# Performance work log

Hardware: AMD Instinct MI355X
Metric: run time of the kernel (lower is better)

Reference implementation:

```python
import jax, jax.numpy as jnp
import numpy as np

N = 50000          # nodes
E = 1_600_000      # edges
R = 16             # num_relations
NB = 4             # num_bases
FIN = 128          # num_node_features
H = 128            # hidden_channels
G = 64             # num graphs in batch
NC = 2             # num_classes


def rgcn_conv(x, edge_index, edge_type, bases, comp, root, bias):
    """PyG RGCNConv with basis decomposition, mean aggregation per relation."""
    n = x.shape[0]
    # weight[r] = sum_b comp[r,b] * bases[b]  -> [R, in, out]
    weight = jnp.einsum('rb,bio->rio', comp, bases)
    src, dst = edge_index[0], edge_index[1]
    # segment id combining destination node and relation
    seg = dst * R + edge_type                      # [E]
    msg = x[src]                                   # [E, in] gather
    summed = jax.ops.segment_sum(msg, seg, num_segments=n * R)      # [N*R, in]
    cnt = jax.ops.segment_sum(jnp.ones((msg.shape[0],), x.dtype), seg,
                              num_segments=n * R)                   # [N*R]
    mean = summed / jnp.maximum(cnt, 1.0)[:, None]
    mean = mean.reshape(n, R, -1)                  # [N, R, in]
    out = jnp.einsum('nri,rio->no', mean, weight) + x @ root + bias
    return out


def global_mean_pool(x, batch, num_graphs):
    s = jax.ops.segment_sum(x, batch, num_segments=num_graphs)
    c = jax.ops.segment_sum(jnp.ones((x.shape[0],), x.dtype), batch,
                            num_segments=num_graphs)
    return s / jnp.maximum(c, 1.0)[:, None]


def setup_inputs() -> dict:
    key = jax.random.key(0)
    ks = jax.random.split(key, 24)
    inp = {
        'x': jax.random.normal(ks[0], (N, FIN), jnp.float32),
        'edge_index': jax.random.randint(ks[1], (2, E), 0, N),
        'edge_type': jax.random.randint(ks[2], (E,), 0, R),
        'batch': jnp.sort(jax.random.randint(ks[3], (N,), 0, G)),
        'rel_labels': jax.random.randint(ks[4], (G,), 0, R),
        'drop_prob': 0,
        'rel_emb': jax.random.normal(ks[5], (R, H), jnp.float32),
    }
    s1 = 1.0 / np.sqrt(FIN)
    s2 = 1.0 / np.sqrt(H)
    inp['bases1'] = jax.random.normal(ks[6], (NB, FIN, H), jnp.float32) * s1
    inp['comp1'] = jax.random.normal(ks[7], (R, NB), jnp.float32)
    inp['root1'] = jax.random.normal(ks[8], (FIN, H), jnp.float32) * s1
    inp['bias1'] = jnp.zeros((H,), jnp.float32)
    inp['bases2'] = jax.random.normal(ks[9], (NB, H, H), jnp.float32) * s2
    inp['comp2'] = jax.random.normal(ks[10], (R, NB), jnp.float32)
    inp['root2'] = jax.random.normal(ks[11], (H, H), jnp.float32) * s2
    inp['bias2'] = jnp.zeros((H,), jnp.float32)
    inp['bases3'] = jax.random.normal(ks[12], (NB, H, H), jnp.float32) * s2
    inp['comp3'] = jax.random.normal(ks[13], (R, NB), jnp.float32)
    inp['root3'] = jax.random.normal(ks[14], (H, H), jnp.float32) * s2
    inp['bias3'] = jnp.zeros((H,), jnp.float32)
    inp['lin_w'] = jax.random.normal(ks[15], (2 * H, NC), jnp.float32) * (1.0 / np.sqrt(2 * H))
    inp['lin_b'] = jnp.zeros((NC,), jnp.float32)
    return inp


def reference(x, edge_index, edge_type, batch, rel_labels, drop_prob, rel_emb,
              bases1, comp1, root1, bias1,
              bases2, comp2, root2, bias2,
              bases3, comp3, root3, bias3,
              lin_w, lin_b):
    rel_embs = rel_emb[rel_labels]                               # [G, H]
    h = jax.nn.relu(rgcn_conv(x, edge_index, edge_type, bases1, comp1, root1, bias1))
    h = jax.nn.relu(rgcn_conv(h, edge_index, edge_type, bases2, comp2, root2, bias2))
    h = rgcn_conv(h, edge_index, edge_type, bases3, comp3, root3, bias3)
    pooled = global_mean_pool(h, batch, G)                       # [G, H]
    z = jnp.concatenate([pooled, rel_embs], axis=1)              # [G, 2H]
    # dropout with p=drop_prob in eval mode (reference is deterministic) -> identity
    return z @ lin_w + lin_b                                     # [G, NC]
```

## Files before the change

kernel.cpp:

```cpp
#include <hip/hip_runtime.h>

#define NN 50000
#define EE 1600000
#define RR 16
#define NBASE 4
#define FINF 128
#define HD 128
#define NG 64
#define NCLS 2
#define NRSEG (NN*RR)

typedef __attribute__((ext_vector_type(8))) short short8;
typedef __attribute__((ext_vector_type(4))) float f32x4;
typedef __attribute__((ext_vector_type(2))) float f32x2;
typedef unsigned short u16;
typedef unsigned int u32;
typedef unsigned long long u64;
typedef unsigned char u8;

__device__ __forceinline__ float bflo(u32 u){ return __builtin_bit_cast(float, u << 16); }
__device__ __forceinline__ float bfhi(u32 u){ return __builtin_bit_cast(float, u & 0xFFFF0000u); }
__device__ __forceinline__ u16 f2bf(float f){
  u32 u = __builtin_bit_cast(u32, f);
  u += 0x7FFFu + ((u >> 16) & 1u);
  return (u16)(u >> 16);
}
__device__ __forceinline__ u32 cvt_pk_bf16(float a, float b){
  u32 r;
  asm("v_cvt_pk_bf16_f32 %0, %1, %2" : "=v"(r) : "v"(a), "v"(b));
  return r;
}
__device__ __forceinline__ float fastrcp(float x){
#if __has_builtin(__builtin_amdgcn_rcpf)
  return __builtin_amdgcn_rcpf(x);
#else
  return 1.0f / x;
#endif
}
__device__ __forceinline__ float ldf(const void* p, int i, int isbf){
  return isbf ? bflo((u32)((const u16*)p)[i]) : ((const float*)p)[i];
}

__device__ __forceinline__ float fp8_manual(u32 b){
  u32 s = (b>>7)&1, e = (b>>3)&15, m = b&7;
  float v;
  if (e==0) v = (float)m * 0.001953125f;
  else      v = __builtin_bit_cast(float, ((e+120u)<<23) | (m<<20));
  return s ? -v : v;
}
__device__ __forceinline__ u32 f32_to_fp8_manual(float f){
  u32 u = __builtin_bit_cast(u32, f);
  u32 s = u>>31;
  int e = (int)((u>>23)&0xFF);
  u32 m = u & 0x7FFFFF;
  int ee = e - 120;
  if (ee <= 0) return s<<7;
  u32 m3 = m >> 20, rem = m & 0xFFFFF;
  u32 rnd = (rem > 0x80000u) || (rem == 0x80000u && (m3 & 1));
  m3 += rnd;
  if (m3 == 8){ m3 = 0; ee += 1; }
  if (ee >= 16){ ee = 15; m3 = 6; }
  return (s<<7) | ((u32)ee<<3) | m3;
}
__device__ __forceinline__ void fp8x2_to_f32(u32 v, float& a, float& b){
#if __has_builtin(__builtin_amdgcn_cvt_pk_f32_fp8)
  f32x2 r = __builtin_amdgcn_cvt_pk_f32_fp8((int)v, false);
  a = r[0]; b = r[1];
#else
  a = fp8_manual(v & 0xFF); b = fp8_manual((v>>8)&0xFF);
#endif
}
__device__ __forceinline__ u32 pk_fp8x2(float a, float b){
  a = fminf(fmaxf(a, -448.f), 448.f);
  b = fminf(fmaxf(b, -448.f), 448.f);
#if __has_builtin(__builtin_amdgcn_cvt_pk_fp8_f32)
  return (u32)__builtin_amdgcn_cvt_pk_fp8_f32(a, b, 0, false) & 0xFFFF;
#else
  return f32_to_fp8_manual(a) | (f32_to_fp8_manual(b) << 8);
#endif
}

__global__ void k_detect(const u32* __restrict__ xw, int* __restrict__ flag){
  __shared__ int votes;
  if (threadIdx.x == 0) votes = 0;
  __syncthreads();
  u32 w = xw[threadIdx.x];
  int e = (w >> 7) & 0xFF;
  if (e >= 100 && e <= 129) atomicAdd(&votes, 1);
  __syncthreads();
  if (threadIdx.x == 0) flag[0] = (votes >= 192) ? 1 : 0;
}

__global__ void k_quant(const void* __restrict__ src, u8* __restrict__ dstq,
                        const int* __restrict__ flagp, int* __restrict__ cnt){
  int i = blockIdx.x*256 + threadIdx.x;
  if (i < NRSEG) cnt[i] = 0;
  if (i >= NN*HD/4) return;
  int isbf = flagp[0];
  float v0,v1,v2,v3;
  if (isbf){
    u32 a = ((const u32*)src)[i*2+0], b = ((const u32*)src)[i*2+1];
    v0=bflo(a); v1=bfhi(a); v2=bflo(b); v3=bfhi(b);
  } else {
    float4 f = ((const float4*)src)[i];
    v0=f.x; v1=f.y; v2=f.z; v3=f.w;
  }
  u32 q = pk_fp8x2(v0,v1) | (pk_fp8x2(v2,v3) << 16);
  ((u32*)dstq)[i] = q;
}


__global__ void k_hist(const int* __restrict__ dst, const int* __restrict__ et,
                       int* __restrict__ cnt){
  int e = blockIdx.x*256 + threadIdx.x;
  if (e < EE) atomicAdd(&cnt[et[e]*NN + dst[e]], 1);
}

#define SCB 1024
__global__ __launch_bounds__(SCB) void k_scan1(const int* __restrict__ cnt,
                                               int* __restrict__ off,
                                               int* __restrict__ bsum){
  __shared__ int sh[SCB];
  int tid = threadIdx.x;
  int i = blockIdx.x*SCB + tid;
  int v = (i < NRSEG) ? cnt[i] : 0;
  sh[tid] = v; __syncthreads();
  for (int d=1; d<SCB; d<<=1){
    int t = (tid >= d) ? sh[tid-d] : 0;
    __syncthreads();
    sh[tid] += t;
    __syncthreads();
  }
  if (i < NRSEG) off[i] = sh[tid] - v;
  if (tid == SCB-1) bsum[blockIdx.x] = sh[SCB-1];
}

__global__ __launch_bounds__(1024) void k_scan2(int* __restrict__ bsum, int nb){
  __shared__ int sh[1024];
  __shared__ int carry;
  int tid = threadIdx.x;
  if (tid == 0) carry = 0;
  __syncthreads();
  for (int base=0; base<nb; base+=1024){
    int i = base + tid;
    int v = (i < nb) ? bsum[i] : 0;
    int orig = v;
    sh[tid] = v; __syncthreads();
    for (int d=1; d<1024; d<<=1){
      int t = (tid >= d) ? sh[tid-d] : 0;
      __syncthreads();
      sh[tid] += t;
      __syncthreads();
    }
    int total = sh[1023];
    int excl = sh[tid] - orig + carry;
    if (i < nb) bsum[i] = excl;
    __syncthreads();
    if (tid == 0) carry += total;
    __syncthreads();
  }
}

__global__ __launch_bounds__(SCB) void k_scan3(const int* __restrict__ cnt,
                                               int* __restrict__ off,
                                               const int* __restrict__ bsum){
  int i = blockIdx.x*SCB + threadIdx.x;
  if (i < NRSEG){
    int o = off[i] + bsum[blockIdx.x];
    off[i] = o;
    if (i == NRSEG-1) off[NRSEG] = o + cnt[i];
  }
}

__global__ void k_scatter(const int* __restrict__ src, const int* __restrict__ dst,
                          const int* __restrict__ et, const int* __restrict__ off,
                          int* __restrict__ cnt, int* __restrict__ esrc){
  int e = blockIdx.x*256 + threadIdx.x;
  if (e < EE){
    int seg = et[e]*NN + dst[e];
    int p = atomicSub(&cnt[seg], 1) - 1;
    esrc[off[seg] + p] = src[e] << 7;
  }
}


__global__ void k_weights3(const void* __restrict__ b0, const void* __restrict__ c0,
                           const void* __restrict__ r0,
                           const void* __restrict__ b1, const void* __restrict__ c1,
                           const void* __restrict__ r1,
                           const void* __restrict__ b2, const void* __restrict__ c2,
                           const void* __restrict__ r2,
                           u16* __restrict__ WTf, const int* __restrict__ flagp){
  int gid = blockIdx.x;
  int layer = gid / 1088;
  int blk = gid - layer*1088;
  int idx = blk*256 + threadIdx.x;
  if (idx >= 17*16384) return;
  const void* bases = (layer==0) ? b0 : (layer==1) ? b1 : b2;
  const void* comp  = (layer==0) ? c0 : (layer==1) ? c1 : c2;
  const void* root  = (layer==0) ? r0 : (layer==1) ? r1 : r2;
  u16* W = WTf + (u32)layer * (17*16384);
  int isbf = flagp[0];
  int r = idx >> 14;
  int o = (idx >> 7) & 127;
  int i = idx & 127;
  float v;
  if (r < RR){
    v = 0.f;
    #pragma unroll
    for (int b=0;b<NBASE;b++)
      v += ldf(comp, r*NBASE+b, isbf) * ldf(bases, (b*FINF + i)*HD + o, isbf);
  } else {
    v = ldf(root, i*HD + o, isbf);
  }
  int wv = o >> 5, ct = (o >> 4) & 1, mrow = o & 15;
  int ks = i >> 5, quad = (i >> 3) & 3, j = i & 7;
  int lane = quad*16 + mrow;
  W[(u32)((((r*4+wv)*2+ct)*4+ks)*64 + lane)*8 + j] = f2bf(v);
}


#define TN 32

#define GLD(rg, ei) { u32 voff_ = (u32)__builtin_amdgcn_readlane(eiv, (ei)) + lane2u; \
  asm volatile("global_load_ushort %0, %1, %2" : "=v"(rg) : "v"(voff_), "s"(xq)); }
#define WAITV0 { asm volatile("s_waitcnt vmcnt(0)" ::: "memory"); \
  __builtin_amdgcn_sched_barrier(0); }
#define CNS(rg, k) if ((k) < cnt){ int eg_ = sbeg + (k); \
  while (idx < TN && nbv <= eg_) doflush(); \
  float da_, db_; fp8x2_to_f32(rg, da_, db_); a0 += da_; a1 += db_; }

__global__ __launch_bounds__(256, 4) void k_layer(
    const u8*  __restrict__ xq,
    const u16* __restrict__ WTf,
    const void* __restrict__ bias, const int* __restrict__ off,
    const int* __restrict__ esrc,
    u16* __restrict__ hout,
    u8* __restrict__ hq,
    const int* __restrict__ flagp, int write_bf, int relu)
{
  __shared__ __align__(16) u16 Abuf[4][TN*136];
  __shared__ int soff[RR*(TN+1)];
  int tid = threadIdx.x;
  int n0 = blockIdx.x * TN;
  int isbf_in = flagp[0];

  int wv = tid >> 6;
  int lane = tid & 63;
  u32 lane2u = (u32)(lane << 1);
  int mrow = lane & 15;
  int quad = lane >> 4;

  for (int i = tid; i < RR*(TN+1); i += 256){
    int r = i / (TN+1), k = i - r*(TN+1);
    int n = n0 + k; if (n > NN) n = NN;
    soff[i] = off[r*NN + n];
  }
  __syncthreads();

  f32x4 acc[2][2];
  { f32x4 z = {0.f,0.f,0.f,0.f};
    acc[0][0]=z; acc[0][1]=z; acc[1][0]=z; acc[1][1]=z; }

  for (int t=0; t<4; ++t){
    int r = t*4 + wv;
    {
      int offv = 0;
      if (lane <= TN) offv = soff[r*(TN+1) + lane];
      int wstart = __builtin_amdgcn_readlane(offv, 0);
      int wend   = __builtin_amdgcn_readlane(offv, TN);
      int blen = wend - wstart;

      float a0 = 0.f, a1 = 0.f;
      int idx = 0;
      int cb = wstart;
      int nbv = __builtin_amdgcn_readlane(offv, 1);
      u16* abase = Abuf[wv] + lane*2;

      auto doflush = [&](){
        int cnt_ = nbv - cb;
        float cf = (float)(cnt_ > 0 ? cnt_ : 1);
        float inv = fastrcp(cf);
        *(u32*)(abase + idx*136) = cvt_pk_bf16(a0*inv, a1*inv);
        a0 = 0.f; a1 = 0.f;
        cb = nbv; idx++;
        if (idx < TN) nbv = __builtin_amdgcn_readlane(offv, idx+1);
      };

      if (blen > 0 && blen <= 128){
        int c0 = blen - 1;
        int eiv0 = esrc[wstart + (lane < c0 ? lane : c0)];
        int eiv1 = 0;
        if (blen > 64){
          int c1 = blen - 65;
          eiv1 = esrc[wstart + 64 + (lane < c1 ? lane : c1)];
        }

        auto batch32 = [&](int eiv, int lb, int sbeg, int cnt)
            __attribute__((always_inline)) {
          u32 r0,r1,r2,r3,r4,r5,r6,r7,r8,r9,r10,r11,r12,r13,r14,r15,
              r16,r17,r18,r19,r20,r21,r22,r23,r24,r25,r26,r27,r28,r29,r30,r31;
          GLD(r0, lb+0) GLD(r1, lb+1) GLD(r2, lb+2) GLD(r3, lb+3)
          GLD(r4, lb+4) GLD(r5, lb+5) GLD(r6, lb+6) GLD(r7, lb+7)
          if (cnt > 8){
            GLD(r8, lb+8)  GLD(r9, lb+9)  GLD(r10, lb+10) GLD(r11, lb+11)
            GLD(r12, lb+12) GLD(r13, lb+13) GLD(r14, lb+14) GLD(r15, lb+15)
          }
          if (cnt > 16){
            GLD(r16, lb+16) GLD(r17, lb+17) GLD(r18, lb+18) GLD(r19, lb+19)
            GLD(r20, lb+20) GLD(r21, lb+21) GLD(r22, lb+22) GLD(r23, lb+23)
          }
          if (cnt > 24){
            GLD(r24, lb+24) GLD(r25, lb+25) GLD(r26, lb+26) GLD(r27, lb+27)
            GLD(r28, lb+28) GLD(r29, lb+29) GLD(r30, lb+30) GLD(r31, lb+31)
          }
          WAITV0
          CNS(r0, 0) CNS(r1, 1) CNS(r2, 2) CNS(r3, 3)
          CNS(r4, 4) CNS(r5, 5) CNS(r6, 6) CNS(r7, 7)
          CNS(r8, 8) CNS(r9, 9) CNS(r10, 10) CNS(r11, 11)
          CNS(r12, 12) CNS(r13, 13) CNS(r14, 14) CNS(r15, 15)
          CNS(r16, 16) CNS(r17, 17) CNS(r18, 18) CNS(r19, 19)
          CNS(r20, 20) CNS(r21, 21) CNS(r22, 22) CNS(r23, 23)
          CNS(r24, 24) CNS(r25, 25) CNS(r26, 26) CNS(r27, 27)
          CNS(r28, 28) CNS(r29, 29) CNS(r30, 30) CNS(r31, 31)
        };

        int cnt0 = blen < 64 ? blen : 64;
        int cA = cnt0 < 32 ? cnt0 : 32;
        batch32(eiv0, 0, wstart, cA);
        if (cnt0 > 32) batch32(eiv0, 32, wstart + 32, cnt0 - 32);
        if (blen > 64){
          int cnt1 = blen - 64;
          int cB = cnt1 < 32 ? cnt1 : 32;
          batch32(eiv1, 0, wstart + 64, cB);
          if (cnt1 > 32) batch32(eiv1, 32, wstart + 96, cnt1 - 32);
        }
      } else if (blen > 0){
        for (int e = wstart; e < wend; ++e){
          int sid = __builtin_amdgcn_readfirstlane(esrc[e]);
          while (idx < TN && nbv <= e) doflush();
          float da, db;
          fp8x2_to_f32((u32)*(const u16*)(xq + (u32)sid + lane2u), da, db);
          a0 += da; a1 += db;
        }
      }
      while (idx < TN) doflush();
    }
    __syncthreads();
    #pragma unroll
    for (int rloc=0; rloc<4; ++rloc){
      int rr = t*4 + rloc;
      const u16* Bp = WTf + (u32)(((rr*4 + wv)*2)*4*64)*8 + (u32)lane*8;
      short8 bf[2][4];
      #pragma unroll
      for (int ct=0; ct<2; ++ct)
        #pragma unroll
        for (int ks=0; ks<4; ++ks)
          bf[ct][ks] = *(const short8*)(Bp + (u32)(ct*4 + ks)*64*8);
      #pragma unroll
      for (int mt=0; mt<2; ++mt){
        #pragma unroll
        for (int ks=0; ks<4; ++ks){
          short8 af = *(const short8*)(Abuf[rloc] + (mt*16 + mrow)*136 + ks*32 + quad*8);
          #pragma unroll
          for (int ct=0; ct<2; ++ct)
            acc[mt][ct] = __builtin_amdgcn_mfma_f32_16x16x32_bf16(af, bf[ct][ks], acc[mt][ct], 0, 0, 0);
        }
      }
    }
    __syncthreads();
  }
  {
    const u16* Bp = WTf + (u32)(((16*4 + wv)*2)*4*64)*8 + (u32)lane*8;
    short8 bf[2][4];
    #pragma unroll
    for (int ct=0; ct<2; ++ct)
      #pragma unroll
      for (int ks=0; ks<4; ++ks)
        bf[ct][ks] = *(const short8*)(Bp + (u32)(ct*4 + ks)*64*8);
    #pragma unroll
    for (int mt=0; mt<2; ++mt){
      const u8* xrow = xq + (u32)(n0 + mt*16 + mrow)*HD;
      #pragma unroll
      for (int ks=0; ks<4; ++ks){
        u32 lo = *(const u32*)(xrow + ks*32 + quad*8);
        u32 hi = *(const u32*)(xrow + ks*32 + quad*8 + 4);
        float f0,f1,f2,f3,f4,f5,f6,f7;
        fp8x2_to_f32(lo & 0xFFFFu, f0, f1);
        fp8x2_to_f32(lo >> 16,     f2, f3);
        fp8x2_to_f32(hi & 0xFFFFu, f4, f5);
        fp8x2_to_f32(hi >> 16,     f6, f7);
        union { short8 v; u32 w[4]; } u;
        u.w[0] = cvt_pk_bf16(f0,f1); u.w[1] = cvt_pk_bf16(f2,f3);
        u.w[2] = cvt_pk_bf16(f4,f5); u.w[3] = cvt_pk_bf16(f6,f7);
        #pragma unroll
        for (int ct=0; ct<2; ++ct)
          acc[mt][ct] = __builtin_amdgcn_mfma_f32_16x16x32_bf16(u.v, bf[ct][ks], acc[mt][ct], 0, 0, 0);
      }
    }
  }
  #pragma unroll
  for (int mt=0; mt<2; ++mt){
    #pragma unroll
    for (int ct=0; ct<2; ++ct){
      int col = wv*32 + ct*16 + mrow;
      float bv = ldf(bias, col, isbf_in);
      #pragma unroll
      for (int rg=0; rg<4; ++rg){
        int n = n0 + mt*16 + quad*4 + rg;
        if (n < NN){
          float v = acc[mt][ct][rg] + bv;
          if (relu) v = fmaxf(v, 0.f);
          if (!(v == v)) v = 0.f;
          if (write_bf) hout[(u32)(n*HD + col)] = f2bf(v);
          else          hq[(u32)(n*HD + col)] = (u8)(pk_fp8x2(v, 0.f) & 0xFF);
        }
      }
    }
  }
}


__global__ __launch_bounds__(1024) void k_pool_head(
    const u16* __restrict__ h, const int* __restrict__ batch,
    const int* __restrict__ rlab, const void* __restrict__ rel_emb,
    const void* __restrict__ lin_w, const void* __restrict__ lin_b,
    void* __restrict__ out, const int* __restrict__ flagp)
{
  int g = blockIdx.x;
  int isbf = flagp[0];
  __shared__ int bounds[2];
  __shared__ float psum[8][128];
  __shared__ float red[4];
  if (threadIdx.x == 0){
    int lo=0, hi=NN;
    while (lo < hi){ int m=(lo+hi)>>1; if (batch[m] < g) lo=m+1; else hi=m; }
    bounds[0] = lo;
    int lo2=lo, hi2=NN;
    while (lo2 < hi2){ int m=(lo2+hi2)>>1; if (batch[m] < g+1) lo2=m+1; else hi2=m; }
    bounds[1] = lo2;
  }
  __syncthreads();
  int lo = bounds[0], hi = bounds[1];
  int f = threadIdx.x & 127;
  int s = threadIdx.x >> 7;
  float acc = 0.f;
  for (int n = lo + s; n < hi; n += 8) acc += bflo((u32)h[(u32)(n*HD + f)]);
  psum[s][f] = acc;
  __syncthreads();
  if (threadIdx.x < 128){
    int cn = hi - lo;
    float tot = 0.f;
    #pragma unroll
    for (int k=0;k<8;k++) tot += psum[k][f];
    float pooled = tot / (float)(cn > 0 ? cn : 1);
    int rl = rlab[g];
    float re = ldf(rel_emb, rl*HD + f, isbf);
    float v0 = pooled * ldf(lin_w, f*NCLS+0, isbf) + re * ldf(lin_w, (HD+f)*NCLS+0, isbf);
    float v1 = pooled * ldf(lin_w, f*NCLS+1, isbf) + re * ldf(lin_w, (HD+f)*NCLS+1, isbf);
    #pragma unroll
    for (int o=32;o>0;o>>=1){ v0 += __shfl_down(v0,o); v1 += __shfl_down(v1,o); }
    int ln = threadIdx.x & 63, wvv = threadIdx.x >> 6;
    if (ln == 0){ red[wvv*2] = v0; red[wvv*2+1] = v1; }
  }
  __syncthreads();
  if (threadIdx.x == 0){
    float o0 = red[0] + red[2] + ldf(lin_b, 0, isbf);
    float o1 = red[1] + red[3] + ldf(lin_b, 1, isbf);
    if (isbf){
      ((u16*)out)[g*NCLS+0] = f2bf(o0);
      ((u16*)out)[g*NCLS+1] = f2bf(o1);
    } else {
      ((float*)out)[g*NCLS+0] = o0;
      ((float*)out)[g*NCLS+1] = o1;
    }
  }
}


extern "C" void kernel_launch(void* const* d_in, const int* in_sizes, int n_in,
                              void* d_out, int out_size, void* d_ws, size_t ws_size,
                              hipStream_t stream)
{
  (void)in_sizes; (void)n_in; (void)out_size; (void)ws_size;
  const void* x      = d_in[0];
  const int* eidx    = (const int*)d_in[1];
  const int* etype   = (const int*)d_in[2];
  const int* batch   = (const int*)d_in[3];
  const int* rlab    = (const int*)d_in[4];
  const void* rel_emb = d_in[6];
  const void* basesA[3] = {d_in[7],  d_in[11], d_in[15]};
  const void* compA[3]  = {d_in[8],  d_in[12], d_in[16]};
  const void* rootA[3]  = {d_in[9],  d_in[13], d_in[17]};
  const void* biasA[3]  = {d_in[10], d_in[14], d_in[18]};
  const void* lin_w  = d_in[19];
  const void* lin_b  = d_in[20];

  char* p = (char*)d_ws;
  auto alloc = [&](size_t bytes)->char*{ char* r = p; p += (bytes + 255) & ~(size_t)255; return r; };
  int*   flag   = (int*)  alloc(256);
  int*   off    = (int*)  alloc((size_t)(NRSEG+1)*4);
  int*   esrc   = (int*)  alloc((size_t)(EE+64)*4);
  u16*   WTf    = (u16*)  alloc((size_t)3*17*16384*2);
  u8*    xq     = (u8*)   alloc((size_t)NN*HD);
  u8*    h1q    = (u8*)   alloc((size_t)NN*HD);
  u8*    h2q    = (u8*)   alloc((size_t)NN*HD);
  u16*   h3     = (u16*)  alloc((size_t)NN*HD*2);
  int*   cnt    = (int*)h3;
  int*   bsum   = (int*)((char*)h3 + (size_t)NRSEG*4);

  const int* src_in = eidx;
  const int* dst_in = eidx + EE;

  const int nscan = (NRSEG + SCB - 1) / SCB;

  k_detect <<<1, 256, 0, stream>>>((const u32*)x, flag);
  k_quant  <<<(NN*HD/4 + 255)/256, 256, 0, stream>>>(x, xq, flag, cnt);
  k_hist   <<<EE/256, 256, 0, stream>>>(dst_in, etype, cnt);
  k_scan1  <<<nscan, SCB, 0, stream>>>(cnt, off, bsum);
  k_scan2  <<<1,    1024, 0, stream>>>(bsum, nscan);
  k_scan3  <<<nscan, SCB, 0, stream>>>(cnt, off, bsum);
  k_scatter<<<EE/256, 256, 0, stream>>>(src_in, dst_in, etype, off, cnt, esrc);

  k_weights3<<<3*1088, 256, 0, stream>>>(basesA[0], compA[0], rootA[0],
                                         basesA[1], compA[1], rootA[1],
                                         basesA[2], compA[2], rootA[2],
                                         WTf, flag);

  const int nblk = (NN + TN - 1) / TN;
  u16* W0 = WTf;
  u16* W1 = WTf + (size_t)1*17*16384;
  u16* W2 = WTf + (size_t)2*17*16384;
  k_layer<<<nblk, 256, 0, stream>>>(xq,  W0, biasA[0], off, esrc, (u16*)0, h1q, flag, 0, 1);
  k_layer<<<nblk, 256, 0, stream>>>(h1q, W1, biasA[1], off, esrc, (u16*)0, h2q, flag, 0, 1);
  k_layer<<<nblk, 256, 0, stream>>>(h2q, W2, biasA[2], off, esrc, h3, (u8*)0, flag, 1, 0);

  k_pool_head<<<NG, 1024, 0, stream>>>(h3, batch, rlab, rel_emb, lin_w, lin_b,
                                       d_out, flag);
}
```

Before: 660.8 us.

## Split each relation's gather across two waves with 512-thread layer blocks

The layer kernel now runs 8 waves per block instead of 4. Each pair of waves shares one relation: each wave gathers and mean-aggregates 16 of the 32 destination nodes, then computes one 16-column half of the MFMA output. This doubles gather parallelism and halves the serial per-wave edge walk and per-wave registers, aiming at higher memory-level parallelism. In exchange there are more waves per block with the same shared buffer, and MFMA work per wave halves, so B-fragment loads are duplicated across waves.

```diff
diff --git a/kernel.cpp b/kernel.cpp
--- a/kernel.cpp
+++ b/kernel.cpp
@@ -221,16 +221,17 @@
 
 
 #define TN 32
+#define TNW 16
 
 #define GLD(rg, ei) { u32 voff_ = (u32)__builtin_amdgcn_readlane(eiv, (ei)) + lane2u; \
   asm volatile("global_load_ushort %0, %1, %2" : "=v"(rg) : "v"(voff_), "s"(xq)); }
 #define WAITV0 { asm volatile("s_waitcnt vmcnt(0)" ::: "memory"); \
   __builtin_amdgcn_sched_barrier(0); }
 #define CNS(rg, k) if ((k) < cnt){ int eg_ = sbeg + (k); \
-  while (idx < TN && nbv <= eg_) doflush(); \
+  while (idx < TNW && nbv <= eg_) doflush(); \
   float da_, db_; fp8x2_to_f32(rg, da_, db_); a0 += da_; a1 += db_; }
 
-__global__ __launch_bounds__(256, 4) void k_layer(
+__global__ __launch_bounds__(512, 8) void k_layer(
     const u8*  __restrict__ xq,
     const u16* __restrict__ WTf,
     const void* __restrict__ bias, const int* __restrict__ off,
@@ -245,37 +246,38 @@
   int n0 = blockIdx.x * TN;
   int isbf_in = flagp[0];
 
-  int wv = tid >> 6;
+  int w = tid >> 6;
   int lane = tid & 63;
   u32 lane2u = (u32)(lane << 1);
   int mrow = lane & 15;
   int quad = lane >> 4;
-
-  for (int i = tid; i < RR*(TN+1); i += 256){
+  int cwv  = w >> 1;
+  int half = w & 1;
+
+  for (int i = tid; i < RR*(TN+1); i += 512){
     int r = i / (TN+1), k = i - r*(TN+1);
     int n = n0 + k; if (n > NN) n = NN;
     soff[i] = off[r*NN + n];
   }
   __syncthreads();
 
-  f32x4 acc[2][2];
-  { f32x4 z = {0.f,0.f,0.f,0.f};
-    acc[0][0]=z; acc[0][1]=z; acc[1][0]=z; acc[1][1]=z; }
+  f32x4 acc[2];
+  { f32x4 z = {0.f,0.f,0.f,0.f}; acc[0] = z; acc[1] = z; }
 
   for (int t=0; t<4; ++t){
-    int r = t*4 + wv;
+    int r = t*4 + cwv;
     {
       int offv = 0;
-      if (lane <= TN) offv = soff[r*(TN+1) + lane];
+      if (lane <= TNW) offv = soff[r*(TN+1) + half*TNW + lane];
       int wstart = __builtin_amdgcn_readlane(offv, 0);
-      int wend   = __builtin_amdgcn_readlane(offv, TN);
+      int wend   = __builtin_amdgcn_readlane(offv, TNW);
       int blen = wend - wstart;
 
       float a0 = 0.f, a1 = 0.f;
       int idx = 0;
       int cb = wstart;
       int nbv = __builtin_amdgcn_readlane(offv, 1);
-      u16* abase = Abuf[wv] + lane*2;
+      u16* abase = Abuf[cwv] + (half*TNW)*136 + lane*2;
 
       auto doflush = [&](){
         int cnt_ = nbv - cb;
@@ -284,7 +286,7 @@
         *(u32*)(abase + idx*136) = cvt_pk_bf16(a0*inv, a1*inv);
         a0 = 0.f; a1 = 0.f;
         cb = nbv; idx++;
-        if (idx < TN) nbv = __builtin_amdgcn_readlane(offv, idx+1);
+        if (idx < TNW) nbv = __builtin_amdgcn_readlane(offv, idx+1);
       };
 
       if (blen > 0 && blen <= 128){
@@ -338,46 +340,40 @@
       } else if (blen > 0){
         for (int e = wstart; e < wend; ++e){
           int sid = __builtin_amdgcn_readfirstlane(esrc[e]);
-          while (idx < TN && nbv <= e) doflush();
+          while (idx < TNW && nbv <= e) doflush();
           float da, db;
           fp8x2_to_f32((u32)*(const u16*)(xq + (u32)sid + lane2u), da, db);
           a0 += da; a1 += db;
         }
       }
-      while (idx < TN) doflush();
+      while (idx < TNW) doflush();
     }
     __syncthreads();
     #pragma unroll
     for (int rloc=0; rloc<4; ++rloc){
       int rr = t*4 + rloc;
-      const u16* Bp = WTf + (u32)(((rr*4 + wv)*2)*4*64)*8 + (u32)lane*8;
-      short8 bf[2][4];
+      const u16* Bp = WTf + (u32)((((rr*4 + cwv)*2 + half)*4)*64)*8 + (u32)lane*8;
+      short8 bf[4];
       #pragma unroll
-      for (int ct=0; ct<2; ++ct)
-        #pragma unroll
-        for (int ks=0; ks<4; ++ks)
-          bf[ct][ks] = *(const short8*)(Bp + (u32)(ct*4 + ks)*64*8);
+      for (int ks=0; ks<4; ++ks)
+        bf[ks] = *(const short8*)(Bp + (u32)ks*64*8);
       #pragma unroll
       for (int mt=0; mt<2; ++mt){
         #pragma unroll
         for (int ks=0; ks<4; ++ks){
           short8 af = *(const short8*)(Abuf[rloc] + (mt*16 + mrow)*136 + ks*32 + quad*8);
-          #pragma unroll
-          for (int ct=0; ct<2; ++ct)
-            acc[mt][ct] = __builtin_amdgcn_mfma_f32_16x16x32_bf16(af, bf[ct][ks], acc[mt][ct], 0, 0, 0);
+          acc[mt] = __builtin_amdgcn_mfma_f32_16x16x32_bf16(af, bf[ks], acc[mt], 0, 0, 0);
         }
       }
     }
     __syncthreads();
   }
   {
-    const u16* Bp = WTf + (u32)(((16*4 + wv)*2)*4*64)*8 + (u32)lane*8;
-    short8 bf[2][4];
-    #pragma unroll
-    for (int ct=0; ct<2; ++ct)
-      #pragma unroll
-      for (int ks=0; ks<4; ++ks)
-        bf[ct][ks] = *(const short8*)(Bp + (u32)(ct*4 + ks)*64*8);
+    const u16* Bp = WTf + (u32)((((16*4 + cwv)*2 + half)*4)*64)*8 + (u32)lane*8;
+    short8 bf[4];
+    #pragma unroll
+    for (int ks=0; ks<4; ++ks)
+      bf[ks] = *(const short8*)(Bp + (u32)ks*64*8);
     #pragma unroll
     for (int mt=0; mt<2; ++mt){
       const u8* xrow = xq + (u32)(n0 + mt*16 + mrow)*HD;
@@ -390,26 +386,23 @@
         fp8x2_to_f32(lo >> 16,     f2, f3);
         fp8x2_to_f32(hi & 0xFFFFu, f4, f5);
         fp8x2_to_f32(hi >> 16,     f6, f7);
-        union { short8 v; u32 w[4]; } u;
-        u.w[0] = cvt_pk_bf16(f0,f1); u.w[1] = cvt_pk_bf16(f2,f3);
-        u.w[2] = cvt_pk_bf16(f4,f5); u.w[3] = cvt_pk_bf16(f6,f7);
-        #pragma unroll
-        for (int ct=0; ct<2; ++ct)
-          acc[mt][ct] = __builtin_amdgcn_mfma_f32_16x16x32_bf16(u.v, bf[ct][ks], acc[mt][ct], 0, 0, 0);
+        union { short8 v; u32 wd[4]; } u;
+        u.wd[0] = cvt_pk_bf16(f0,f1); u.wd[1] = cvt_pk_bf16(f2,f3);
+        u.wd[2] = cvt_pk_bf16(f4,f5); u.wd[3] = cvt_pk_bf16(f6,f7);
+        acc[mt] = __builtin_amdgcn_mfma_f32_16x16x32_bf16(u.v, bf[ks], acc[mt], 0, 0, 0);
       }
     }
   }
-  #pragma unroll
-  for (int mt=0; mt<2; ++mt){
-    #pragma unroll
-    for (int ct=0; ct<2; ++ct){
-      int col = wv*32 + ct*16 + mrow;
-      float bv = ldf(bias, col, isbf_in);
+  {
+    int col = cwv*32 + half*16 + mrow;
+    float bv = ldf(bias, col, isbf_in);
+    #pragma unroll
+    for (int mt=0; mt<2; ++mt){
       #pragma unroll
       for (int rg=0; rg<4; ++rg){
         int n = n0 + mt*16 + quad*4 + rg;
         if (n < NN){
-          float v = acc[mt][ct][rg] + bv;
+          float v = acc[mt][rg] + bv;
           if (relu) v = fmaxf(v, 0.f);
           if (!(v == v)) v = 0.f;
           if (write_bf) hout[(u32)(n*HD + col)] = f2bf(v);
@@ -531,9 +524,9 @@
   u16* W0 = WTf;
   u16* W1 = WTf + (size_t)1*17*16384;
   u16* W2 = WTf + (size_t)2*17*16384;
-  k_layer<<<nblk, 256, 0, stream>>>(xq,  W0, biasA[0], off, esrc, (u16*)0, h1q, flag, 0, 1);
-  k_layer<<<nblk, 256, 0, stream>>>(h1q, W1, biasA[1], off, esrc, (u16*)0, h2q, flag, 0, 1);
-  k_layer<<<nblk, 256, 0, stream>>>(h2q, W2, biasA[2], off, esrc, h3, (u8*)0, flag, 1, 0);
+  k_layer<<<nblk, 512, 0, stream>>>(xq,  W0, biasA[0], off, esrc, (u16*)0, h1q, flag, 0, 1);
+  k_layer<<<nblk, 512, 0, stream>>>(h1q, W1, biasA[1], off, esrc, (u16*)0, h2q, flag, 0, 1);
+  k_layer<<<nblk, 512, 0, stream>>>(h2q, W2, biasA[2], off, esrc, h3, (u8*)0, flag, 1, 0);
 
   k_pool_head<<<NG, 1024, 0, stream>>>(h3, batch, rlab, rel_emb, lin_w, lin_b,
                                        d_out, flag);
```

Result: faster. 617.5 us (-6.6%).
